# Kernel tuning notes

Measured on AMD Instinct MI355X. Metric: run time of the kernel, lower is better.

The kernel has to match this reference:

```python
import jax, jax.numpy as jnp
import numpy as np

NUM_CLUSTERS = 32


def setup_inputs() -> dict:
    key = jax.random.key(0)
    k1, k2 = jax.random.split(key)
    B, N, D = 16, 16384, 128
    x = jax.random.normal(k1, (B, N, D), dtype=jnp.float32)
    cluster_ids = jax.random.randint(k2, (B, N), 0, NUM_CLUSTERS, dtype=jnp.int32)
    return {"x": x, "cluster_ids": cluster_ids}


def reference(x, cluster_ids):
    # x: [B, N, D]; cluster_ids: [B, N] int labels in [0, C)
    C = NUM_CLUSTERS
    # One-hot cluster membership: [B, N, C]
    onehot = (cluster_ids[..., None] == jnp.arange(C, dtype=cluster_ids.dtype)).astype(x.dtype)
    counts = onehot.sum(axis=1)                       # [B, C]
    sums = jnp.einsum('bnc,bnd->bcd', onehot, x)      # segment sums [B, C, D]
    # Per-cluster mean; empty clusters -> zero rows (contribute 0 to off-diag Gram)
    means = sums / jnp.maximum(counts, 1.0)[..., None]
    # Pairwise |dot products| between cluster means: [B, C, C]
    gram = jnp.abs(jnp.einsum('bcd,bed->bce', means, means))
    # Strict upper-triangular sum (torch.triu(..., diagonal=1))
    triu_mask = jnp.triu(jnp.ones((C, C), dtype=x.dtype), k=1)
    triu_sum = jnp.sum(gram * triu_mask, axis=(1, 2))  # [B]
    # Number of valid (non-empty) clusters per batch
    valid = jnp.sum(counts > 0, axis=1).astype(x.dtype)
    denom = jnp.where(valid > 1, valid * (valid - 1.0) * 0.5, 1.0)
    return jnp.mean(triu_sum / denom)
```

## Files before the change

### kernel.cpp

```cpp
#include <hip/hip_runtime.h>
#include <hip/hip_bf16.h>

#define BB 16
#define NN 16384
#define DD 128
#define CC 32
#define CHUNKS 32
#define NBLK (BB * CHUNKS)
#define ROWS_PER_BLOCK (NN / CHUNKS)
#define ROWS_PER_WAVE  (ROWS_PER_BLOCK / 4)

#define P_SUMS 0
#define P_CNTS ((size_t)NBLK * CC * DD)
#define LOSSP  (P_CNTS + (size_t)NBLK * CC)
#define CTR    (LOSSP + BB)
#define WS_A_FLOATS (CTR + 1)

__global__ __launch_bounds__(256) void seg_sum_kernel(
    const float* __restrict__ x, const int* __restrict__ ids,
    float* __restrict__ outsums, float* __restrict__ outcnts,
    int* __restrict__ counter, int mode) {
  __shared__ float lsum[4][CC * DD];
  __shared__ float lcnt[CC];
  __shared__ int   lcid[ROWS_PER_BLOCK];

  const int tid  = threadIdx.x;
  const int b    = blockIdx.y;
  const int row0 = blockIdx.x * ROWS_PER_BLOCK;
  const int lane = tid & 63;
  const int w    = tid >> 6;
  const int slot = b * CHUNKS + blockIdx.x;
  const int* __restrict__ idrow = ids + (size_t)b * NN;

  if (tid < CC) lcnt[tid] = 0.f;
  lcid[tid]       = idrow[row0 + tid];
  lcid[tid + 256] = idrow[row0 + tid + 256];
  {
    const float4 z4 = make_float4(0.f, 0.f, 0.f, 0.f);
#pragma unroll
    for (int i = 0; i < 16; ++i)
      *reinterpret_cast<float4*>(&lsum[w][(i * 64 + lane) * 4]) = z4;
  }
  __syncthreads();
  atomicAdd(&lcnt[lcid[tid]], 1.f);
  atomicAdd(&lcnt[lcid[tid + 256]], 1.f);

  const float2* __restrict__ x2 =
      reinterpret_cast<const float2*>(x + (size_t)b * NN * DD);
  const int wbase = w * ROWS_PER_WAVE;
  float* const slab = &lsum[w][0];

  float2 vA[16], vB[16];
  int cA[16], cB[16];

#define LOADG(V, C, g)                                                     \
  {                                                                        \
    _Pragma("unroll") for (int k = 0; k < 16; ++k) {                       \
      const int rl = wbase + (g) * 16 + k;                                 \
      V[k] = x2[(size_t)(row0 + rl) * 64 + lane];                          \
      C[k] = lcid[rl];                                                     \
    }                                                                      \
  }
#define RMWG(V, C)                                                         \
  {                                                                        \
    _Pragma("unroll") for (int k = 0; k < 16; ++k) {                       \
      float2* p = reinterpret_cast<float2*>(&slab[C[k] * DD + 2 * lane]);  \
      float2 old = *p;                                                     \
      *p = make_float2(old.x + V[k].x, old.y + V[k].y);                    \
    }                                                                      \
  }

  LOADG(vA, cA, 0)
#pragma unroll
  for (int i = 0; i < 3; ++i) {
    LOADG(vB, cB, 2 * i + 1)
    RMWG(vA, cA)
    LOADG(vA, cA, 2 * i + 2)
    RMWG(vB, cB)
  }
  LOADG(vB, cB, 7)
  RMWG(vA, cA)
  RMWG(vB, cB)
#undef LOADG
#undef RMWG
  __syncthreads();

  if (mode) {
    float* __restrict__ ps = outsums + (size_t)slot * CC * DD;
#pragma unroll
    for (int it = 0; it < 4; ++it) {
      const int i = (it * 256 + tid) * 4;
      float4 s0 = *reinterpret_cast<const float4*>(&lsum[0][i]);
      float4 s1 = *reinterpret_cast<const float4*>(&lsum[1][i]);
      float4 s2 = *reinterpret_cast<const float4*>(&lsum[2][i]);
      float4 s3 = *reinterpret_cast<const float4*>(&lsum[3][i]);
      float4 r = make_float4(s0.x + s1.x + s2.x + s3.x, s0.y + s1.y + s2.y + s3.y,
                             s0.z + s1.z + s2.z + s3.z, s0.w + s1.w + s2.w + s3.w);
      *reinterpret_cast<float4*>(&ps[i]) = r;
    }
    if (tid < CC) outcnts[slot * CC + tid] = lcnt[tid];
    if (slot == 0 && tid == 0)
      __hip_atomic_store(counter, 0, __ATOMIC_RELAXED, __HIP_MEMORY_SCOPE_AGENT);
  } else {
    float* __restrict__ gs = outsums + (size_t)b * CC * DD;
    for (int i = tid; i < CC * DD; i += 256) {
      float s = lsum[0][i] + lsum[1][i] + lsum[2][i] + lsum[3][i];
      atomicAdd(&gs[i], s);
    }
    if (tid < CC) atomicAdd(&outcnts[b * CC + tid], lcnt[tid]);
  }
}

#define MSTR 132
__global__ __launch_bounds__(512) void finish_fused_kernel(
    const float* __restrict__ psums, const float* __restrict__ pcnts,
    float* __restrict__ lossp, int* __restrict__ counter,
    float* __restrict__ out) {
  __shared__ float mean[CC * MSTR];
  __shared__ float cnt[CC];
  __shared__ float red[512];

  const int b = blockIdx.x;
  const int tid = threadIdx.x;

  if (tid < CC) {
    float cs = 0.f;
#pragma unroll 8
    for (int c = 0; c < CHUNKS; ++c) cs += pcnts[(b * CHUNKS + c) * CC + tid];
    cnt[tid] = cs;
  }

  float4 a0 = make_float4(0.f, 0.f, 0.f, 0.f), a1 = a0;
  const size_t base = (size_t)b * CHUNKS * CC * DD + (size_t)tid * 8;
#pragma unroll 4
  for (int c = 0; c < CHUNKS; ++c) {
    const float4* p = reinterpret_cast<const float4*>(&psums[base + (size_t)c * CC * DD]);
    float4 q0 = p[0], q1 = p[1];
    a0.x += q0.x; a0.y += q0.y; a0.z += q0.z; a0.w += q0.w;
    a1.x += q1.x; a1.y += q1.y; a1.z += q1.z; a1.w += q1.w;
  }
  __syncthreads();

  {
    const int c = tid >> 4;
    const int d0 = (tid & 15) * 8;
    const float inv = 1.f / fmaxf(cnt[c], 1.f);
    float* mrow = &mean[c * MSTR + d0];
    mrow[0] = a0.x * inv; mrow[1] = a0.y * inv; mrow[2] = a0.z * inv; mrow[3] = a0.w * inv;
    mrow[4] = a1.x * inv; mrow[5] = a1.y * inv; mrow[6] = a1.z * inv; mrow[7] = a1.w * inv;
  }
  __syncthreads();

  float acc = 0.f;
  if (tid < (CC * (CC - 1)) / 2) {
    int c = 0, rem = tid;
    while (rem >= (CC - 1 - c)) { rem -= (CC - 1 - c); ++c; }
    int e = c + 1 + rem;
    const float4* mc = reinterpret_cast<const float4*>(&mean[c * MSTR]);
    const float4* me = reinterpret_cast<const float4*>(&mean[e * MSTR]);
    float dot = 0.f;
#pragma unroll 8
    for (int j = 0; j < DD / 4; ++j) {
      float4 u = mc[j], v = me[j];
      dot += u.x * v.x + u.y * v.y + u.z * v.z + u.w * v.w;
    }
    acc = fabsf(dot);
  }

  red[tid] = acc;
  __syncthreads();
  for (int s = 256; s > 0; s >>= 1) {
    if (tid < s) red[tid] += red[tid + s];
    __syncthreads();
  }

  if (tid == 0) {
    float valid = 0.f;
    for (int c = 0; c < CC; ++c) valid += (cnt[c] > 0.f) ? 1.f : 0.f;
    float denom = (valid > 1.f) ? valid * (valid - 1.f) * 0.5f : 1.f;
    float v = red[0] / denom * (1.0f / BB);
    __hip_atomic_store(&lossp[b], v, __ATOMIC_RELAXED, __HIP_MEMORY_SCOPE_AGENT);
    __threadfence();
    int old = __hip_atomic_fetch_add(counter, 1, __ATOMIC_ACQ_REL,
                                     __HIP_MEMORY_SCOPE_AGENT);
    if (old == BB - 1) {
      float s = 0.f;
#pragma unroll
      for (int i = 0; i < BB; ++i)
        s += __hip_atomic_load(&lossp[i], __ATOMIC_RELAXED,
                               __HIP_MEMORY_SCOPE_AGENT);
      out[0] = s;
    }
  }
}

__global__ __launch_bounds__(512) void finish_kernel_b(
    const float* __restrict__ gsums, const float* __restrict__ gcounts,
    float* __restrict__ out) {
  __shared__ float mean[CC * MSTR];
  __shared__ float cnt[CC];
  __shared__ float red[512];

  const int b = blockIdx.x;
  const int tid = threadIdx.x;

  if (tid < CC) cnt[tid] = gcounts[b * CC + tid];
  __syncthreads();

  for (int i = tid; i < CC * DD; i += 512) {
    int c = i >> 7;
    int d = i & 127;
    mean[c * MSTR + d] = gsums[(size_t)b * CC * DD + i] / fmaxf(cnt[c], 1.f);
  }
  __syncthreads();

  float acc = 0.f;
  if (tid < (CC * (CC - 1)) / 2) {
    int c = 0, rem = tid;
    while (rem >= (CC - 1 - c)) { rem -= (CC - 1 - c); ++c; }
    int e = c + 1 + rem;
    const float4* mc = reinterpret_cast<const float4*>(&mean[c * MSTR]);
    const float4* me = reinterpret_cast<const float4*>(&mean[e * MSTR]);
    float dot = 0.f;
#pragma unroll 8
    for (int j = 0; j < DD / 4; ++j) {
      float4 u = mc[j], v = me[j];
      dot += u.x * v.x + u.y * v.y + u.z * v.z + u.w * v.w;
    }
    acc = fabsf(dot);
  }

  red[tid] = acc;
  __syncthreads();
  for (int s = 256; s > 0; s >>= 1) {
    if (tid < s) red[tid] += red[tid + s];
    __syncthreads();
  }

  if (tid == 0) {
    float valid = 0.f;
    for (int c = 0; c < CC; ++c) valid += (cnt[c] > 0.f) ? 1.f : 0.f;
    float denom = (valid > 1.f) ? valid * (valid - 1.f) * 0.5f : 1.f;
    atomicAdd(out, red[0] / denom * (1.0f / BB));
  }
}

extern "C" void kernel_launch(void* const* d_in, const int* in_sizes, int n_in,
                              void* d_out, int out_size, void* d_ws, size_t ws_size,
                              hipStream_t stream) {
  const float* x   = (const float*)d_in[0];
  const int*   ids = (const int*)d_in[1];
  float* out = (float*)d_out;
  float* ws  = (float*)d_ws;

  dim3 grid1(CHUNKS, BB);
  if (ws_size >= WS_A_FLOATS * sizeof(float)) {
    float* psums = ws + P_SUMS;
    float* pcnts = ws + P_CNTS;
    float* lossp = ws + LOSSP;
    int*   ctr   = (int*)(ws + CTR);
    seg_sum_kernel<<<grid1, 256, 0, stream>>>(x, ids, psums, pcnts, ctr, 1);
    finish_fused_kernel<<<BB, 512, 0, stream>>>(psums, pcnts, lossp, ctr, out);
  } else {
    float* gsums   = ws;
    float* gcounts = gsums + (size_t)BB * CC * DD;
    const size_t wsb = ((size_t)BB * CC * DD + (size_t)BB * CC) * sizeof(float);
    hipMemsetAsync(d_ws, 0, wsb, stream);
    hipMemsetAsync(d_out, 0, sizeof(float), stream);
    seg_sum_kernel<<<grid1, 256, 0, stream>>>(x, ids, gsums, gcounts, nullptr, 0);
    finish_kernel_b<<<BB, 512, 0, stream>>>(gsums, gcounts, out);
  }
}
```

Baseline: 39.16 us.

## Compute segment sums with bf16 split-precision MFMA one-hot matmul

Replaces the per-row LDS read-modify-write accumulation with a one-hot matrix multiply on MFMA units. Each fp32 x value is split into high and low bf16 parts, giving two MFMAs per tile that approximate fp32 accuracy. The block grows to 512 threads with register accumulators, so the LDS is written only once at the end rather than per row. This removes LDS RMW traffic and bank conflicts, at the cost of extra conversion ALU work and a small precision loss from the bf16 hi/lo split.

```diff
diff --git a/kernel.cpp b/kernel.cpp
--- a/kernel.cpp
+++ b/kernel.cpp
@@ -8,7 +8,6 @@
 #define CHUNKS 32
 #define NBLK (BB * CHUNKS)
 #define ROWS_PER_BLOCK (NN / CHUNKS)
-#define ROWS_PER_WAVE  (ROWS_PER_BLOCK / 4)
 
 #define P_SUMS 0
 #define P_CNTS ((size_t)NBLK * CC * DD)
@@ -16,10 +15,20 @@
 #define CTR    (LOSSP + BB)
 #define WS_A_FLOATS (CTR + 1)
 
-__global__ __launch_bounds__(256) void seg_sum_kernel(
+typedef float f32x16 __attribute__((ext_vector_type(16)));
+typedef short short8 __attribute__((ext_vector_type(8)));
+
+union FragU { short8 s; unsigned int u[4]; };
+union BfU { __hip_bfloat162 h; unsigned int u; };
+
+static __device__ inline float asfloat_u(unsigned int u) {
+  union { unsigned int u; float f; } c; c.u = u; return c.f;
+}
+
+__global__ __launch_bounds__(512, 4) void seg_mfma_kernel(
     const float* __restrict__ x, const int* __restrict__ ids,
     float* __restrict__ outsums, float* __restrict__ outcnts,
-    int* __restrict__ counter, int mode) {
+    int* __restrict__ counter) {
   __shared__ float lsum[4][CC * DD];
   __shared__ float lcnt[CC];
   __shared__ int   lcid[ROWS_PER_BLOCK];
@@ -29,86 +38,108 @@
   const int row0 = blockIdx.x * ROWS_PER_BLOCK;
   const int lane = tid & 63;
   const int w    = tid >> 6;
+  const int q    = w >> 1;
+  const int hh   = w & 1;
+  const int half = lane >> 5;
+  const int ln31 = lane & 31;
   const int slot = b * CHUNKS + blockIdx.x;
   const int* __restrict__ idrow = ids + (size_t)b * NN;
 
   if (tid < CC) lcnt[tid] = 0.f;
-  lcid[tid]       = idrow[row0 + tid];
-  lcid[tid + 256] = idrow[row0 + tid + 256];
-  {
-    const float4 z4 = make_float4(0.f, 0.f, 0.f, 0.f);
-#pragma unroll
-    for (int i = 0; i < 16; ++i)
-      *reinterpret_cast<float4*>(&lsum[w][(i * 64 + lane) * 4]) = z4;
-  }
+  lcid[tid] = idrow[row0 + tid];
   __syncthreads();
   atomicAdd(&lcnt[lcid[tid]], 1.f);
-  atomicAdd(&lcnt[lcid[tid + 256]], 1.f);
-
-  const float2* __restrict__ x2 =
-      reinterpret_cast<const float2*>(x + (size_t)b * NN * DD);
-  const int wbase = w * ROWS_PER_WAVE;
-  float* const slab = &lsum[w][0];
-
-  float2 vA[16], vB[16];
-  int cA[16], cB[16];
-
-#define LOADG(V, C, g)                                                     \
-  {                                                                        \
-    _Pragma("unroll") for (int k = 0; k < 16; ++k) {                       \
-      const int rl = wbase + (g) * 16 + k;                                 \
-      V[k] = x2[(size_t)(row0 + rl) * 64 + lane];                          \
-      C[k] = lcid[rl];                                                     \
-    }                                                                      \
-  }
-#define RMWG(V, C)                                                         \
-  {                                                                        \
-    _Pragma("unroll") for (int k = 0; k < 16; ++k) {                       \
-      float2* p = reinterpret_cast<float2*>(&slab[C[k] * DD + 2 * lane]);  \
-      float2 old = *p;                                                     \
-      *p = make_float2(old.x + V[k].x, old.y + V[k].y);                    \
-    }                                                                      \
-  }
-
-  LOADG(vA, cA, 0)
+
+  f32x16 acc0, acc1;
+#pragma unroll
+  for (int i = 0; i < 16; ++i) { acc0[i] = 0.f; acc1[i] = 0.f; }
+
+  const float* __restrict__ p0 =
+      x + ((size_t)b * NN + row0 + q * 128 + half * 8) * DD + hh * 64 + ln31;
+  const int kb0 = q * 128 + half * 8;
+
+  float bufA[16], bufB[16];
+
+#define LOADCH(BUF, j)                                                      \
+  {                                                                         \
+    _Pragma("unroll") for (int e = 0; e < 8; ++e) {                         \
+      BUF[e]     = p0[((j) * 16 + e) * DD];                                 \
+      BUF[8 + e] = p0[((j) * 16 + e) * DD + 32];                            \
+    }                                                                       \
+  }
+
+#define PROCCH(BUF, j)                                                      \
+  {                                                                         \
+    FragU af;                                                               \
+    _Pragma("unroll") for (int i = 0; i < 4; ++i) {                         \
+      const int c0 = lcid[kb0 + (j) * 16 + 2 * i];                          \
+      const int c1 = lcid[kb0 + (j) * 16 + 2 * i + 1];                      \
+      const unsigned int lo = (c0 == ln31) ? 0x3F80u : 0u;                  \
+      const unsigned int hi = (c1 == ln31) ? 0x3F80u : 0u;                  \
+      af.u[i] = lo | (hi << 16);                                            \
+    }                                                                       \
+    FragU bh0, bl0, bh1, bl1;                                               \
+    _Pragma("unroll") for (int i = 0; i < 4; ++i) {                         \
+      {                                                                     \
+        const float a0 = BUF[2 * i], a1 = BUF[2 * i + 1];                   \
+        BfU hv; hv.h = __float22bfloat162_rn(make_float2(a0, a1));          \
+        const float f0 = asfloat_u(hv.u << 16);                             \
+        const float f1 = asfloat_u(hv.u & 0xFFFF0000u);                     \
+        BfU lv; lv.h = __float22bfloat162_rn(make_float2(a0 - f0, a1 - f1));\
+        bh0.u[i] = hv.u; bl0.u[i] = lv.u;                                   \
+      }                                                                     \
+      {                                                                     \
+        const float a0 = BUF[8 + 2 * i], a1 = BUF[8 + 2 * i + 1];           \
+        BfU hv; hv.h = __float22bfloat162_rn(make_float2(a0, a1));          \
+        const float f0 = asfloat_u(hv.u << 16);                             \
+        const float f1 = asfloat_u(hv.u & 0xFFFF0000u);                     \
+        BfU lv; lv.h = __float22bfloat162_rn(make_float2(a0 - f0, a1 - f1));\
+        bh1.u[i] = hv.u; bl1.u[i] = lv.u;                                   \
+      }                                                                     \
+    }                                                                       \
+    acc0 = __builtin_amdgcn_mfma_f32_32x32x16_bf16(af.s, bh0.s, acc0, 0, 0, 0); \
+    acc0 = __builtin_amdgcn_mfma_f32_32x32x16_bf16(af.s, bl0.s, acc0, 0, 0, 0); \
+    acc1 = __builtin_amdgcn_mfma_f32_32x32x16_bf16(af.s, bh1.s, acc1, 0, 0, 0); \
+    acc1 = __builtin_amdgcn_mfma_f32_32x32x16_bf16(af.s, bl1.s, acc1, 0, 0, 0); \
+  }
+
+  LOADCH(bufA, 0)
 #pragma unroll
   for (int i = 0; i < 3; ++i) {
-    LOADG(vB, cB, 2 * i + 1)
-    RMWG(vA, cA)
-    LOADG(vA, cA, 2 * i + 2)
-    RMWG(vB, cB)
-  }
-  LOADG(vB, cB, 7)
-  RMWG(vA, cA)
-  RMWG(vB, cB)
-#undef LOADG
-#undef RMWG
-  __syncthreads();
-
-  if (mode) {
-    float* __restrict__ ps = outsums + (size_t)slot * CC * DD;
-#pragma unroll
-    for (int it = 0; it < 4; ++it) {
-      const int i = (it * 256 + tid) * 4;
-      float4 s0 = *reinterpret_cast<const float4*>(&lsum[0][i]);
-      float4 s1 = *reinterpret_cast<const float4*>(&lsum[1][i]);
-      float4 s2 = *reinterpret_cast<const float4*>(&lsum[2][i]);
-      float4 s3 = *reinterpret_cast<const float4*>(&lsum[3][i]);
-      float4 r = make_float4(s0.x + s1.x + s2.x + s3.x, s0.y + s1.y + s2.y + s3.y,
-                             s0.z + s1.z + s2.z + s3.z, s0.w + s1.w + s2.w + s3.w);
-      *reinterpret_cast<float4*>(&ps[i]) = r;
-    }
-    if (tid < CC) outcnts[slot * CC + tid] = lcnt[tid];
-    if (slot == 0 && tid == 0)
-      __hip_atomic_store(counter, 0, __ATOMIC_RELAXED, __HIP_MEMORY_SCOPE_AGENT);
-  } else {
-    float* __restrict__ gs = outsums + (size_t)b * CC * DD;
-    for (int i = tid; i < CC * DD; i += 256) {
-      float s = lsum[0][i] + lsum[1][i] + lsum[2][i] + lsum[3][i];
-      atomicAdd(&gs[i], s);
-    }
-    if (tid < CC) atomicAdd(&outcnts[b * CC + tid], lcnt[tid]);
-  }
+    LOADCH(bufB, 2 * i + 1)
+    PROCCH(bufA, 2 * i)
+    LOADCH(bufA, 2 * i + 2)
+    PROCCH(bufB, 2 * i + 1)
+  }
+  LOADCH(bufB, 7)
+  PROCCH(bufA, 6)
+  PROCCH(bufB, 7)
+#undef LOADCH
+#undef PROCCH
+
+#pragma unroll
+  for (int r = 0; r < 16; ++r) {
+    const int m = (r & 3) + 8 * (r >> 2) + 4 * half;
+    lsum[q][m * DD + hh * 64 + ln31]      = acc0[r];
+    lsum[q][m * DD + hh * 64 + 32 + ln31] = acc1[r];
+  }
+  __syncthreads();
+
+  float* __restrict__ ps = outsums + (size_t)slot * CC * DD;
+#pragma unroll
+  for (int it = 0; it < 2; ++it) {
+    const int i = (it * 512 + tid) * 4;
+    float4 s0 = *reinterpret_cast<const float4*>(&lsum[0][i]);
+    float4 s1 = *reinterpret_cast<const float4*>(&lsum[1][i]);
+    float4 s2 = *reinterpret_cast<const float4*>(&lsum[2][i]);
+    float4 s3 = *reinterpret_cast<const float4*>(&lsum[3][i]);
+    float4 r = make_float4(s0.x + s1.x + s2.x + s3.x, s0.y + s1.y + s2.y + s3.y,
+                           s0.z + s1.z + s2.z + s3.z, s0.w + s1.w + s2.w + s3.w);
+    *reinterpret_cast<float4*>(&ps[i]) = r;
+  }
+  if (tid < CC) outcnts[slot * CC + tid] = lcnt[tid];
+  if (slot == 0 && tid == 0)
+    __hip_atomic_store(counter, 0, __ATOMIC_RELAXED, __HIP_MEMORY_SCOPE_AGENT);
 }
 
 #define MSTR 132
@@ -194,6 +225,64 @@
   }
 }
 
+#define ROWS_PER_WAVE_B 128
+__global__ __launch_bounds__(256) void seg_sum_rmw_kernel(
+    const float* __restrict__ x, const int* __restrict__ ids,
+    float* __restrict__ gsums, float* __restrict__ gcounts) {
+  __shared__ float lsum[4][CC * DD];
+  __shared__ float lcnt[CC];
+  __shared__ int   lcid[ROWS_PER_BLOCK];
+
+  const int tid  = threadIdx.x;
+  const int b    = blockIdx.y;
+  const int row0 = blockIdx.x * ROWS_PER_BLOCK;
+  const int lane = tid & 63;
+  const int w    = tid >> 6;
+  const int* __restrict__ idrow = ids + (size_t)b * NN;
+
+  if (tid < CC) lcnt[tid] = 0.f;
+  lcid[tid]       = idrow[row0 + tid];
+  lcid[tid + 256] = idrow[row0 + tid + 256];
+  {
+    const float4 z4 = make_float4(0.f, 0.f, 0.f, 0.f);
+#pragma unroll
+    for (int i = 0; i < 16; ++i)
+      *reinterpret_cast<float4*>(&lsum[w][(i * 64 + lane) * 4]) = z4;
+  }
+  __syncthreads();
+  atomicAdd(&lcnt[lcid[tid]], 1.f);
+  atomicAdd(&lcnt[lcid[tid + 256]], 1.f);
+
+  const float2* __restrict__ x2 =
+      reinterpret_cast<const float2*>(x + (size_t)b * NN * DD);
+  const int wbase = w * ROWS_PER_WAVE_B;
+  float* const slab = &lsum[w][0];
+
+  for (int g = 0; g < ROWS_PER_WAVE_B / 8; ++g) {
+    float2 v[8]; int cid[8];
+#pragma unroll
+    for (int k = 0; k < 8; ++k) {
+      const int rl = wbase + g * 8 + k;
+      v[k]   = x2[(size_t)(row0 + rl) * 64 + lane];
+      cid[k] = lcid[rl];
+    }
+#pragma unroll
+    for (int k = 0; k < 8; ++k) {
+      float2* p = reinterpret_cast<float2*>(&slab[cid[k] * DD + 2 * lane]);
+      float2 old = *p;
+      *p = make_float2(old.x + v[k].x, old.y + v[k].y);
+    }
+  }
+  __syncthreads();
+
+  float* __restrict__ gs = gsums + (size_t)b * CC * DD;
+  for (int i = tid; i < CC * DD; i += 256) {
+    float s = lsum[0][i] + lsum[1][i] + lsum[2][i] + lsum[3][i];
+    atomicAdd(&gs[i], s);
+  }
+  if (tid < CC) atomicAdd(&gcounts[b * CC + tid], lcnt[tid]);
+}
+
 __global__ __launch_bounds__(512) void finish_kernel_b(
     const float* __restrict__ gsums, const float* __restrict__ gcounts,
     float* __restrict__ out) {
@@ -259,7 +348,7 @@
     float* pcnts = ws + P_CNTS;
     float* lossp = ws + LOSSP;
     int*   ctr   = (int*)(ws + CTR);
-    seg_sum_kernel<<<grid1, 256, 0, stream>>>(x, ids, psums, pcnts, ctr, 1);
+    seg_mfma_kernel<<<grid1, 512, 0, stream>>>(x, ids, psums, pcnts, ctr);
     finish_fused_kernel<<<BB, 512, 0, stream>>>(psums, pcnts, lossp, ctr, out);
   } else {
     float* gsums   = ws;
@@ -267,7 +356,7 @@
     const size_t wsb = ((size_t)BB * CC * DD + (size_t)BB * CC) * sizeof(float);
     hipMemsetAsync(d_ws, 0, wsb, stream);
     hipMemsetAsync(d_out, 0, sizeof(float), stream);
-    seg_sum_kernel<<<grid1, 256, 0, stream>>>(x, ids, gsums, gcounts, nullptr, 0);
+    seg_sum_rmw_kernel<<<grid1, 256, 0, stream>>>(x, ids, gsums, gcounts);
     finish_kernel_b<<<BB, 512, 0, stream>>>(gsums, gcounts, out);
   }
 }
```

Result: no change. 39.23 us (+0.2%).

## Split partial-sum reduction across 256 blocks with per-batch last-block finish

Applied to the files above, without the earlier changes.

The finishing kernel previously used only 16 blocks, each reducing 32 chunk partials of a whole batch. Now 256 blocks each reduce a 256-element slice and write the result to a reduced buffer. A per-batch atomic counter picks the last-arriving block, which then computes the means, the pairwise Gram sum and the final loss. This spreads the memory-bound partial reduction over many more CUs, at the cost of an extra global round-trip and more atomics. The fallback path is moved into a separate kernel without the mode flag.

```diff
diff --git a/kernel.cpp b/kernel.cpp
--- a/kernel.cpp
+++ b/kernel.cpp
@@ -12,14 +12,17 @@
 
 #define P_SUMS 0
 #define P_CNTS ((size_t)NBLK * CC * DD)
-#define LOSSP  (P_CNTS + (size_t)NBLK * CC)
-#define CTR    (LOSSP + BB)
-#define WS_A_FLOATS (CTR + 1)
+#define R_SUMS (P_CNTS + (size_t)NBLK * CC)
+#define R_CNTS (R_SUMS + (size_t)BB * CC * DD)
+#define LOSSP  (R_CNTS + (size_t)BB * CC)
+#define BCTR   (LOSSP + BB)
+#define GCTR   (BCTR + BB)
+#define WS_A_FLOATS (GCTR + 1)
 
 __global__ __launch_bounds__(256) void seg_sum_kernel(
     const float* __restrict__ x, const int* __restrict__ ids,
     float* __restrict__ outsums, float* __restrict__ outcnts,
-    int* __restrict__ counter, int mode) {
+    int* __restrict__ bctr, int* __restrict__ gctr) {
   __shared__ float lsum[4][CC * DD];
   __shared__ float lcnt[CC];
   __shared__ int   lcid[ROWS_PER_BLOCK];
@@ -85,36 +88,179 @@
 #undef RMWG
   __syncthreads();
 
-  if (mode) {
-    float* __restrict__ ps = outsums + (size_t)slot * CC * DD;
-#pragma unroll
-    for (int it = 0; it < 4; ++it) {
-      const int i = (it * 256 + tid) * 4;
-      float4 s0 = *reinterpret_cast<const float4*>(&lsum[0][i]);
-      float4 s1 = *reinterpret_cast<const float4*>(&lsum[1][i]);
-      float4 s2 = *reinterpret_cast<const float4*>(&lsum[2][i]);
-      float4 s3 = *reinterpret_cast<const float4*>(&lsum[3][i]);
-      float4 r = make_float4(s0.x + s1.x + s2.x + s3.x, s0.y + s1.y + s2.y + s3.y,
-                             s0.z + s1.z + s2.z + s3.z, s0.w + s1.w + s2.w + s3.w);
-      *reinterpret_cast<float4*>(&ps[i]) = r;
-    }
-    if (tid < CC) outcnts[slot * CC + tid] = lcnt[tid];
-    if (slot == 0 && tid == 0)
-      __hip_atomic_store(counter, 0, __ATOMIC_RELAXED, __HIP_MEMORY_SCOPE_AGENT);
-  } else {
-    float* __restrict__ gs = outsums + (size_t)b * CC * DD;
-    for (int i = tid; i < CC * DD; i += 256) {
-      float s = lsum[0][i] + lsum[1][i] + lsum[2][i] + lsum[3][i];
-      atomicAdd(&gs[i], s);
-    }
-    if (tid < CC) atomicAdd(&outcnts[b * CC + tid], lcnt[tid]);
+  float* __restrict__ ps = outsums + (size_t)slot * CC * DD;
+#pragma unroll
+  for (int it = 0; it < 4; ++it) {
+    const int i = (it * 256 + tid) * 4;
+    float4 s0 = *reinterpret_cast<const float4*>(&lsum[0][i]);
+    float4 s1 = *reinterpret_cast<const float4*>(&lsum[1][i]);
+    float4 s2 = *reinterpret_cast<const float4*>(&lsum[2][i]);
+    float4 s3 = *reinterpret_cast<const float4*>(&lsum[3][i]);
+    float4 r = make_float4(s0.x + s1.x + s2.x + s3.x, s0.y + s1.y + s2.y + s3.y,
+                           s0.z + s1.z + s2.z + s3.z, s0.w + s1.w + s2.w + s3.w);
+    *reinterpret_cast<float4*>(&ps[i]) = r;
+  }
+  if (tid < CC) outcnts[slot * CC + tid] = lcnt[tid];
+  if (slot == 0) {
+    if (tid < BB)
+      __hip_atomic_store(&bctr[tid], 0, __ATOMIC_RELAXED, __HIP_MEMORY_SCOPE_AGENT);
+    if (tid == BB)
+      __hip_atomic_store(gctr, 0, __ATOMIC_RELAXED, __HIP_MEMORY_SCOPE_AGENT);
   }
 }
 
 #define MSTR 132
-__global__ __launch_bounds__(512) void finish_fused_kernel(
+__global__ __launch_bounds__(256) void finish2_kernel(
     const float* __restrict__ psums, const float* __restrict__ pcnts,
-    float* __restrict__ lossp, int* __restrict__ counter,
+    float* __restrict__ rsums, float* __restrict__ rcnts,
+    float* __restrict__ lossp, int* __restrict__ bctr, int* __restrict__ gctr,
+    float* __restrict__ out) {
+  __shared__ float mean[CC * MSTR];
+  __shared__ float cnt[CC];
+  __shared__ float red[256];
+  __shared__ int   lastF;
+
+  const int j = blockIdx.x;
+  const int b = j >> 4;
+  const int p = j & 15;
+  const int tid = threadIdx.x;
+
+  {
+    const int e = p * 256 + tid;
+    const float* base = psums + (size_t)b * CHUNKS * CC * DD + e;
+    float s = 0.f;
+#pragma unroll 8
+    for (int c = 0; c < CHUNKS; ++c) s += base[(size_t)c * CC * DD];
+    rsums[(size_t)b * CC * DD + e] = s;
+  }
+  if (p == 0 && tid < CC) {
+    float cs = 0.f;
+#pragma unroll 8
+    for (int c = 0; c < CHUNKS; ++c) cs += pcnts[(b * CHUNKS + c) * CC + tid];
+    rcnts[b * CC + tid] = cs;
+  }
+  __threadfence();
+  __syncthreads();
+  if (tid == 0) {
+    int old = __hip_atomic_fetch_add(&bctr[b], 1, __ATOMIC_ACQ_REL,
+                                     __HIP_MEMORY_SCOPE_AGENT);
+    lastF = (old == 15);
+  }
+  __syncthreads();
+  if (!lastF) return;
+  __threadfence();
+
+  if (tid < CC) cnt[tid] = rcnts[b * CC + tid];
+  __syncthreads();
+  for (int i = tid; i < CC * DD; i += 256) {
+    int c = i >> 7;
+    int d = i & 127;
+    mean[c * MSTR + d] = rsums[(size_t)b * CC * DD + i] / fmaxf(cnt[c], 1.f);
+  }
+  __syncthreads();
+
+  float acc = 0.f;
+  for (int pp = tid; pp < (CC * (CC - 1)) / 2; pp += 256) {
+    int c = 0, rem = pp;
+    while (rem >= (CC - 1 - c)) { rem -= (CC - 1 - c); ++c; }
+    int e = c + 1 + rem;
+    const float4* mc = reinterpret_cast<const float4*>(&mean[c * MSTR]);
+    const float4* me = reinterpret_cast<const float4*>(&mean[e * MSTR]);
+    float dot = 0.f;
+#pragma unroll 8
+    for (int jj = 0; jj < DD / 4; ++jj) {
+      float4 u = mc[jj], v = me[jj];
+      dot += u.x * v.x + u.y * v.y + u.z * v.z + u.w * v.w;
+    }
+    acc += fabsf(dot);
+  }
+  red[tid] = acc;
+  __syncthreads();
+  for (int s = 128; s > 0; s >>= 1) {
+    if (tid < s) red[tid] += red[tid + s];
+    __syncthreads();
+  }
+
+  if (tid == 0) {
+    float valid = 0.f;
+    for (int c = 0; c < CC; ++c) valid += (cnt[c] > 0.f) ? 1.f : 0.f;
+    float denom = (valid > 1.f) ? valid * (valid - 1.f) * 0.5f : 1.f;
+    float v = red[0] / denom * (1.0f / BB);
+    __hip_atomic_store(&lossp[b], v, __ATOMIC_RELAXED, __HIP_MEMORY_SCOPE_AGENT);
+    __threadfence();
+    int old = __hip_atomic_fetch_add(gctr, 1, __ATOMIC_ACQ_REL,
+                                     __HIP_MEMORY_SCOPE_AGENT);
+    if (old == BB - 1) {
+      __threadfence();
+      float s = 0.f;
+#pragma unroll
+      for (int i = 0; i < BB; ++i)
+        s += __hip_atomic_load(&lossp[i], __ATOMIC_RELAXED,
+                               __HIP_MEMORY_SCOPE_AGENT);
+      out[0] = s;
+    }
+  }
+}
+
+__global__ __launch_bounds__(256) void seg_sum_rmw_b(
+    const float* __restrict__ x, const int* __restrict__ ids,
+    float* __restrict__ gsums, float* __restrict__ gcounts) {
+  __shared__ float lsum[4][CC * DD];
+  __shared__ float lcnt[CC];
+  __shared__ int   lcid[ROWS_PER_BLOCK];
+
+  const int tid  = threadIdx.x;
+  const int b    = blockIdx.y;
+  const int row0 = blockIdx.x * ROWS_PER_BLOCK;
+  const int lane = tid & 63;
+  const int w    = tid >> 6;
+  const int* __restrict__ idrow = ids + (size_t)b * NN;
+
+  if (tid < CC) lcnt[tid] = 0.f;
+  lcid[tid]       = idrow[row0 + tid];
+  lcid[tid + 256] = idrow[row0 + tid + 256];
+  {
+    const float4 z4 = make_float4(0.f, 0.f, 0.f, 0.f);
+#pragma unroll
+    for (int i = 0; i < 16; ++i)
+      *reinterpret_cast<float4*>(&lsum[w][(i * 64 + lane) * 4]) = z4;
+  }
+  __syncthreads();
+  atomicAdd(&lcnt[lcid[tid]], 1.f);
+  atomicAdd(&lcnt[lcid[tid + 256]], 1.f);
+
+  const float2* __restrict__ x2 =
+      reinterpret_cast<const float2*>(x + (size_t)b * NN * DD);
+  const int wbase = w * ROWS_PER_WAVE;
+  float* const slab = &lsum[w][0];
+
+  for (int g = 0; g < ROWS_PER_WAVE / 8; ++g) {
+    float2 v[8]; int cid[8];
+#pragma unroll
+    for (int k = 0; k < 8; ++k) {
+      const int rl = wbase + g * 8 + k;
+      v[k]   = x2[(size_t)(row0 + rl) * 64 + lane];
+      cid[k] = lcid[rl];
+    }
+#pragma unroll
+    for (int k = 0; k < 8; ++k) {
+      float2* p = reinterpret_cast<float2*>(&slab[cid[k] * DD + 2 * lane]);
+      float2 old = *p;
+      *p = make_float2(old.x + v[k].x, old.y + v[k].y);
+    }
+  }
+  __syncthreads();
+
+  float* __restrict__ gs = gsums + (size_t)b * CC * DD;
+  for (int i = tid; i < CC * DD; i += 256) {
+    float s = lsum[0][i] + lsum[1][i] + lsum[2][i] + lsum[3][i];
+    atomicAdd(&gs[i], s);
+  }
+  if (tid < CC) atomicAdd(&gcounts[b * CC + tid], lcnt[tid]);
+}
+
+__global__ __launch_bounds__(512) void finish_kernel_b(
+    const float* __restrict__ gsums, const float* __restrict__ gcounts,
     float* __restrict__ out) {
   __shared__ float mean[CC * MSTR];
   __shared__ float cnt[CC];
@@ -123,31 +269,12 @@
   const int b = blockIdx.x;
   const int tid = threadIdx.x;
 
-  if (tid < CC) {
-    float cs = 0.f;
-#pragma unroll 8
-    for (int c = 0; c < CHUNKS; ++c) cs += pcnts[(b * CHUNKS + c) * CC + tid];
-    cnt[tid] = cs;
-  }
-
-  float4 a0 = make_float4(0.f, 0.f, 0.f, 0.f), a1 = a0;
-  const size_t base = (size_t)b * CHUNKS * CC * DD + (size_t)tid * 8;
-#pragma unroll 4
-  for (int c = 0; c < CHUNKS; ++c) {
-    const float4* p = reinterpret_cast<const float4*>(&psums[base + (size_t)c * CC * DD]);
-    float4 q0 = p[0], q1 = p[1];
-    a0.x += q0.x; a0.y += q0.y; a0.z += q0.z; a0.w += q0.w;
-    a1.x += q1.x; a1.y += q1.y; a1.z += q1.z; a1.w += q1.w;
-  }
-  __syncthreads();
-
-  {
-    const int c = tid >> 4;
-    const int d0 = (tid & 15) * 8;
-    const float inv = 1.f / fmaxf(cnt[c], 1.f);
-    float* mrow = &mean[c * MSTR + d0];
-    mrow[0] = a0.x * inv; mrow[1] = a0.y * inv; mrow[2] = a0.z * inv; mrow[3] = a0.w * inv;
-    mrow[4] = a1.x * inv; mrow[5] = a1.y * inv; mrow[6] = a1.z * inv; mrow[7] = a1.w * inv;
+  if (tid < CC) cnt[tid] = gcounts[b * CC + tid];
+  __syncthreads();
+  for (int i = tid; i < CC * DD; i += 512) {
+    int c = i >> 7;
+    int d = i & 127;
+    mean[c * MSTR + d] = gsums[(size_t)b * CC * DD + i] / fmaxf(cnt[c], 1.f);
   }
   __syncthreads();
 
@@ -160,83 +287,18 @@
     const float4* me = reinterpret_cast<const float4*>(&mean[e * MSTR]);
     float dot = 0.f;
 #pragma unroll 8
-    for (int j = 0; j < DD / 4; ++j) {
-      float4 u = mc[j], v = me[j];
+    for (int jj = 0; jj < DD / 4; ++jj) {
+      float4 u = mc[jj], v = me[jj];
       dot += u.x * v.x + u.y * v.y + u.z * v.z + u.w * v.w;
     }
     acc = fabsf(dot);
   }
-
   red[tid] = acc;
   __syncthreads();
   for (int s = 256; s > 0; s >>= 1) {
     if (tid < s) red[tid] += red[tid + s];
     __syncthreads();
   }
-
-  if (tid == 0) {
-    float valid = 0.f;
-    for (int c = 0; c < CC; ++c) valid += (cnt[c] > 0.f) ? 1.f : 0.f;
-    float denom = (valid > 1.f) ? valid * (valid - 1.f) * 0.5f : 1.f;
-    float v = red[0] / denom * (1.0f / BB);
-    __hip_atomic_store(&lossp[b], v, __ATOMIC_RELAXED, __HIP_MEMORY_SCOPE_AGENT);
-    __threadfence();
-    int old = __hip_atomic_fetch_add(counter, 1, __ATOMIC_ACQ_REL,
-                                     __HIP_MEMORY_SCOPE_AGENT);
-    if (old == BB - 1) {
-      float s = 0.f;
-#pragma unroll
-      for (int i = 0; i < BB; ++i)
-        s += __hip_atomic_load(&lossp[i], __ATOMIC_RELAXED,
-                               __HIP_MEMORY_SCOPE_AGENT);
-      out[0] = s;
-    }
-  }
-}
-
-__global__ __launch_bounds__(512) void finish_kernel_b(
-    const float* __restrict__ gsums, const float* __restrict__ gcounts,
-    float* __restrict__ out) {
-  __shared__ float mean[CC * MSTR];
-  __shared__ float cnt[CC];
-  __shared__ float red[512];
-
-  const int b = blockIdx.x;
-  const int tid = threadIdx.x;
-
-  if (tid < CC) cnt[tid] = gcounts[b * CC + tid];
-  __syncthreads();
-
-  for (int i = tid; i < CC * DD; i += 512) {
-    int c = i >> 7;
-    int d = i & 127;
-    mean[c * MSTR + d] = gsums[(size_t)b * CC * DD + i] / fmaxf(cnt[c], 1.f);
-  }
-  __syncthreads();
-
-  float acc = 0.f;
-  if (tid < (CC * (CC - 1)) / 2) {
-    int c = 0, rem = tid;
-    while (rem >= (CC - 1 - c)) { rem -= (CC - 1 - c); ++c; }
-    int e = c + 1 + rem;
-    const float4* mc = reinterpret_cast<const float4*>(&mean[c * MSTR]);
-    const float4* me = reinterpret_cast<const float4*>(&mean[e * MSTR]);
-    float dot = 0.f;
-#pragma unroll 8
-    for (int j = 0; j < DD / 4; ++j) {
-      float4 u = mc[j], v = me[j];
-      dot += u.x * v.x + u.y * v.y + u.z * v.z + u.w * v.w;
-    }
-    acc = fabsf(dot);
-  }
-
-  red[tid] = acc;
-  __syncthreads();
-  for (int s = 256; s > 0; s >>= 1) {
-    if (tid < s) red[tid] += red[tid + s];
-    __syncthreads();
-  }
-
   if (tid == 0) {
     float valid = 0.f;
     for (int c = 0; c < CC; ++c) valid += (cnt[c] > 0.f) ? 1.f : 0.f;
@@ -257,17 +319,21 @@
   if (ws_size >= WS_A_FLOATS * sizeof(float)) {
     float* psums = ws + P_SUMS;
     float* pcnts = ws + P_CNTS;
+    float* rsums = ws + R_SUMS;
+    float* rcnts = ws + R_CNTS;
     float* lossp = ws + LOSSP;
-    int*   ctr   = (int*)(ws + CTR);
-    seg_sum_kernel<<<grid1, 256, 0, stream>>>(x, ids, psums, pcnts, ctr, 1);
-    finish_fused_kernel<<<BB, 512, 0, stream>>>(psums, pcnts, lossp, ctr, out);
+    int*   bctr  = (int*)(ws + BCTR);
+    int*   gctr  = (int*)(ws + GCTR);
+    seg_sum_kernel<<<grid1, 256, 0, stream>>>(x, ids, psums, pcnts, bctr, gctr);
+    finish2_kernel<<<NBLK / 2, 256, 0, stream>>>(psums, pcnts, rsums, rcnts,
+                                                 lossp, bctr, gctr, out);
   } else {
     float* gsums   = ws;
     float* gcounts = gsums + (size_t)BB * CC * DD;
     const size_t wsb = ((size_t)BB * CC * DD + (size_t)BB * CC) * sizeof(float);
     hipMemsetAsync(d_ws, 0, wsb, stream);
     hipMemsetAsync(d_out, 0, sizeof(float), stream);
-    seg_sum_kernel<<<grid1, 256, 0, stream>>>(x, ids, gsums, gcounts, nullptr, 0);
+    seg_sum_rmw_b<<<grid1, 256, 0, stream>>>(x, ids, gsums, gcounts);
     finish_kernel_b<<<BB, 512, 0, stream>>>(gsums, gcounts, out);
   }
 }
```

Result: slower. 67.07 us (+71.3%).

## Split feature dimension across wave pairs with 512-thread blocks in segment-sum kernel

Applied to the files above, without the earlier changes.

The segment-sum kernel now uses 512 threads, 8 waves. Each wave pair splits the 128-wide feature row into two 64-float halves, so a wave keeps a 32x64 shared-memory slab instead of a full 32x128 one. Shared memory per block stays the same while waves per block double, and fewer registers per thread (8 scalar loads per group instead of 16 float2) allow a higher occupancy hint. The fallback path moves to a separate kernel with the old layout, and a thread fence is added before the final reduction. Scalar per-lane loads replace float2 loads, which may reduce per-request memory efficiency.

```diff
diff --git a/kernel.cpp b/kernel.cpp
--- a/kernel.cpp
+++ b/kernel.cpp
@@ -8,19 +8,18 @@
 #define CHUNKS 32
 #define NBLK (BB * CHUNKS)
 #define ROWS_PER_BLOCK (NN / CHUNKS)
-#define ROWS_PER_WAVE  (ROWS_PER_BLOCK / 4)
 
 #define P_SUMS 0
 #define P_CNTS ((size_t)NBLK * CC * DD)
 #define LOSSP  (P_CNTS + (size_t)NBLK * CC)
-#define CTR    (LOSSP + BB)
-#define WS_A_FLOATS (CTR + 1)
-
-__global__ __launch_bounds__(256) void seg_sum_kernel(
+#define GCTR   (LOSSP + BB)
+#define WS_A_FLOATS (GCTR + 1)
+
+__global__ __launch_bounds__(512, 4) void seg_sum_kernel(
     const float* __restrict__ x, const int* __restrict__ ids,
     float* __restrict__ outsums, float* __restrict__ outcnts,
-    int* __restrict__ counter, int mode) {
-  __shared__ float lsum[4][CC * DD];
+    int* __restrict__ gctr) {
+  __shared__ float slab[8][CC * 64];
   __shared__ float lcnt[CC];
   __shared__ int   lcid[ROWS_PER_BLOCK];
 
@@ -29,92 +28,80 @@
   const int row0 = blockIdx.x * ROWS_PER_BLOCK;
   const int lane = tid & 63;
   const int w    = tid >> 6;
+  const int rr   = w >> 1;
+  const int h    = w & 1;
   const int slot = b * CHUNKS + blockIdx.x;
   const int* __restrict__ idrow = ids + (size_t)b * NN;
 
   if (tid < CC) lcnt[tid] = 0.f;
-  lcid[tid]       = idrow[row0 + tid];
-  lcid[tid + 256] = idrow[row0 + tid + 256];
+  lcid[tid] = idrow[row0 + tid];
   {
     const float4 z4 = make_float4(0.f, 0.f, 0.f, 0.f);
 #pragma unroll
-    for (int i = 0; i < 16; ++i)
-      *reinterpret_cast<float4*>(&lsum[w][(i * 64 + lane) * 4]) = z4;
+    for (int i = 0; i < 8; ++i)
+      *reinterpret_cast<float4*>(&slab[w][(i * 64 + lane) * 4]) = z4;
   }
   __syncthreads();
   atomicAdd(&lcnt[lcid[tid]], 1.f);
-  atomicAdd(&lcnt[lcid[tid + 256]], 1.f);
-
-  const float2* __restrict__ x2 =
-      reinterpret_cast<const float2*>(x + (size_t)b * NN * DD);
-  const int wbase = w * ROWS_PER_WAVE;
-  float* const slab = &lsum[w][0];
-
-  float2 vA[16], vB[16];
-  int cA[16], cB[16];
+
+  const float* __restrict__ p0 =
+      x + ((size_t)b * NN + row0 + rr * 128) * DD + h * 64 + lane;
+  const int kb0 = rr * 128;
+  float* const sl = &slab[w][0];
+
+  float vA[8], vB[8];
+  int cA[8], cB[8];
 
 #define LOADG(V, C, g)                                                     \
   {                                                                        \
-    _Pragma("unroll") for (int k = 0; k < 16; ++k) {                       \
-      const int rl = wbase + (g) * 16 + k;                                 \
-      V[k] = x2[(size_t)(row0 + rl) * 64 + lane];                          \
-      C[k] = lcid[rl];                                                     \
+    _Pragma("unroll") for (int k = 0; k < 8; ++k) {                        \
+      V[k] = p0[((g) * 8 + k) * DD];                                       \
+      C[k] = lcid[kb0 + (g) * 8 + k];                                      \
     }                                                                      \
   }
 #define RMWG(V, C)                                                         \
   {                                                                        \
-    _Pragma("unroll") for (int k = 0; k < 16; ++k) {                       \
-      float2* p = reinterpret_cast<float2*>(&slab[C[k] * DD + 2 * lane]);  \
-      float2 old = *p;                                                     \
-      *p = make_float2(old.x + V[k].x, old.y + V[k].y);                    \
+    _Pragma("unroll") for (int k = 0; k < 8; ++k) {                        \
+      float* p = &sl[C[k] * 64 + lane];                                    \
+      *p = *p + V[k];                                                      \
     }                                                                      \
   }
 
   LOADG(vA, cA, 0)
 #pragma unroll
-  for (int i = 0; i < 3; ++i) {
+  for (int i = 0; i < 7; ++i) {
     LOADG(vB, cB, 2 * i + 1)
     RMWG(vA, cA)
     LOADG(vA, cA, 2 * i + 2)
     RMWG(vB, cB)
   }
-  LOADG(vB, cB, 7)
+  LOADG(vB, cB, 15)
   RMWG(vA, cA)
   RMWG(vB, cB)
 #undef LOADG
 #undef RMWG
   __syncthreads();
 
-  if (mode) {
-    float* __restrict__ ps = outsums + (size_t)slot * CC * DD;
-#pragma unroll
-    for (int it = 0; it < 4; ++it) {
-      const int i = (it * 256 + tid) * 4;
-      float4 s0 = *reinterpret_cast<const float4*>(&lsum[0][i]);
-      float4 s1 = *reinterpret_cast<const float4*>(&lsum[1][i]);
-      float4 s2 = *reinterpret_cast<const float4*>(&lsum[2][i]);
-      float4 s3 = *reinterpret_cast<const float4*>(&lsum[3][i]);
-      float4 r = make_float4(s0.x + s1.x + s2.x + s3.x, s0.y + s1.y + s2.y + s3.y,
-                             s0.z + s1.z + s2.z + s3.z, s0.w + s1.w + s2.w + s3.w);
-      *reinterpret_cast<float4*>(&ps[i]) = r;
-    }
-    if (tid < CC) outcnts[slot * CC + tid] = lcnt[tid];
-    if (slot == 0 && tid == 0)
-      __hip_atomic_store(counter, 0, __ATOMIC_RELAXED, __HIP_MEMORY_SCOPE_AGENT);
-  } else {
-    float* __restrict__ gs = outsums + (size_t)b * CC * DD;
-    for (int i = tid; i < CC * DD; i += 256) {
-      float s = lsum[0][i] + lsum[1][i] + lsum[2][i] + lsum[3][i];
-      atomicAdd(&gs[i], s);
-    }
-    if (tid < CC) atomicAdd(&outcnts[b * CC + tid], lcnt[tid]);
-  }
+  float* __restrict__ ps = outsums + (size_t)slot * CC * DD;
+#pragma unroll
+  for (int it = 0; it < 8; ++it) {
+    const int idx = it * 512 + tid;
+    const int c  = idx >> 7;
+    const int r  = idx & 127;
+    const int h2 = r >> 6;
+    const int j  = r & 63;
+    const int o  = c * 64 + j;
+    ps[idx] = slab[h2][o] + slab[2 + h2][o] + slab[4 + h2][o] + slab[6 + h2][o];
+  }
+  if (tid < CC) outcnts[slot * CC + tid] = lcnt[tid];
+  if (slot == 0 && tid == 0)
+    __hip_atomic_store(gctr, 0, __ATOMIC_RELAXED, __HIP_MEMORY_SCOPE_AGENT);
 }
 
 #define MSTR 132
 __global__ __launch_bounds__(512) void finish_fused_kernel(
     const float* __restrict__ psums, const float* __restrict__ pcnts,
-    float* __restrict__ lossp, int* __restrict__ counter,
+    float* __restrict__ lossp, int* __restrict__ gctr,
     float* __restrict__ out) {
   __shared__ float mean[CC * MSTR];
   __shared__ float cnt[CC];
@@ -181,9 +168,10 @@
     float v = red[0] / denom * (1.0f / BB);
     __hip_atomic_store(&lossp[b], v, __ATOMIC_RELAXED, __HIP_MEMORY_SCOPE_AGENT);
     __threadfence();
-    int old = __hip_atomic_fetch_add(counter, 1, __ATOMIC_ACQ_REL,
+    int old = __hip_atomic_fetch_add(gctr, 1, __ATOMIC_ACQ_REL,
                                      __HIP_MEMORY_SCOPE_AGENT);
     if (old == BB - 1) {
+      __threadfence();
       float s = 0.f;
 #pragma unroll
       for (int i = 0; i < BB; ++i)
@@ -192,6 +180,64 @@
       out[0] = s;
     }
   }
+}
+
+#define ROWS_PER_WAVE_B 128
+__global__ __launch_bounds__(256) void seg_sum_rmw_b(
+    const float* __restrict__ x, const int* __restrict__ ids,
+    float* __restrict__ gsums, float* __restrict__ gcounts) {
+  __shared__ float lsum[4][CC * DD];
+  __shared__ float lcnt[CC];
+  __shared__ int   lcid[ROWS_PER_BLOCK];
+
+  const int tid  = threadIdx.x;
+  const int b    = blockIdx.y;
+  const int row0 = blockIdx.x * ROWS_PER_BLOCK;
+  const int lane = tid & 63;
+  const int w    = tid >> 6;
+  const int* __restrict__ idrow = ids + (size_t)b * NN;
+
+  if (tid < CC) lcnt[tid] = 0.f;
+  lcid[tid]       = idrow[row0 + tid];
+  lcid[tid + 256] = idrow[row0 + tid + 256];
+  {
+    const float4 z4 = make_float4(0.f, 0.f, 0.f, 0.f);
+#pragma unroll
+    for (int i = 0; i < 16; ++i)
+      *reinterpret_cast<float4*>(&lsum[w][(i * 64 + lane) * 4]) = z4;
+  }
+  __syncthreads();
+  atomicAdd(&lcnt[lcid[tid]], 1.f);
+  atomicAdd(&lcnt[lcid[tid + 256]], 1.f);
+
+  const float2* __restrict__ x2 =
+      reinterpret_cast<const float2*>(x + (size_t)b * NN * DD);
+  const int wbase = w * ROWS_PER_WAVE_B;
+  float* const slab = &lsum[w][0];
+
+  for (int g = 0; g < ROWS_PER_WAVE_B / 8; ++g) {
+    float2 v[8]; int cid[8];
+#pragma unroll
+    for (int k = 0; k < 8; ++k) {
+      const int rl = wbase + g * 8 + k;
+      v[k]   = x2[(size_t)(row0 + rl) * 64 + lane];
+      cid[k] = lcid[rl];
+    }
+#pragma unroll
+    for (int k = 0; k < 8; ++k) {
+      float2* p = reinterpret_cast<float2*>(&slab[cid[k] * DD + 2 * lane]);
+      float2 old = *p;
+      *p = make_float2(old.x + v[k].x, old.y + v[k].y);
+    }
+  }
+  __syncthreads();
+
+  float* __restrict__ gs = gsums + (size_t)b * CC * DD;
+  for (int i = tid; i < CC * DD; i += 256) {
+    float s = lsum[0][i] + lsum[1][i] + lsum[2][i] + lsum[3][i];
+    atomicAdd(&gs[i], s);
+  }
+  if (tid < CC) atomicAdd(&gcounts[b * CC + tid], lcnt[tid]);
 }
 
 __global__ __launch_bounds__(512) void finish_kernel_b(
@@ -206,7 +252,6 @@
 
   if (tid < CC) cnt[tid] = gcounts[b * CC + tid];
   __syncthreads();
-
   for (int i = tid; i < CC * DD; i += 512) {
     int c = i >> 7;
     int d = i & 127;
@@ -223,20 +268,18 @@
     const float4* me = reinterpret_cast<const float4*>(&mean[e * MSTR]);
     float dot = 0.f;
 #pragma unroll 8
-    for (int j = 0; j < DD / 4; ++j) {
-      float4 u = mc[j], v = me[j];
+    for (int jj = 0; jj < DD / 4; ++jj) {
+      float4 u = mc[jj], v = me[jj];
       dot += u.x * v.x + u.y * v.y + u.z * v.z + u.w * v.w;
     }
     acc = fabsf(dot);
   }
-
   red[tid] = acc;
   __syncthreads();
   for (int s = 256; s > 0; s >>= 1) {
     if (tid < s) red[tid] += red[tid + s];
     __syncthreads();
   }
-
   if (tid == 0) {
     float valid = 0.f;
     for (int c = 0; c < CC; ++c) valid += (cnt[c] > 0.f) ? 1.f : 0.f;
@@ -258,16 +301,16 @@
     float* psums = ws + P_SUMS;
     float* pcnts = ws + P_CNTS;
     float* lossp = ws + LOSSP;
-    int*   ctr   = (int*)(ws + CTR);
-    seg_sum_kernel<<<grid1, 256, 0, stream>>>(x, ids, psums, pcnts, ctr, 1);
-    finish_fused_kernel<<<BB, 512, 0, stream>>>(psums, pcnts, lossp, ctr, out);
+    int*   gctr  = (int*)(ws + GCTR);
+    seg_sum_kernel<<<grid1, 512, 0, stream>>>(x, ids, psums, pcnts, gctr);
+    finish_fused_kernel<<<BB, 512, 0, stream>>>(psums, pcnts, lossp, gctr, out);
   } else {
     float* gsums   = ws;
     float* gcounts = gsums + (size_t)BB * CC * DD;
     const size_t wsb = ((size_t)BB * CC * DD + (size_t)BB * CC) * sizeof(float);
     hipMemsetAsync(d_ws, 0, wsb, stream);
     hipMemsetAsync(d_out, 0, sizeof(float), stream);
-    seg_sum_kernel<<<grid1, 256, 0, stream>>>(x, ids, gsums, gcounts, nullptr, 0);
+    seg_sum_rmw_b<<<grid1, 256, 0, stream>>>(x, ids, gsums, gcounts);
     finish_kernel_b<<<BB, 512, 0, stream>>>(gsums, gcounts, out);
   }
 }
```

New measurement: 39.35 us. No clear change (+0.5%).
